# Performance work log

Hardware: AMD Instinct MI355X
Metric: run time of the kernel (lower is better)

The kernel has to match this reference:

```python
import jax, jax.numpy as jnp
import numpy as np

B, H, C, W = 16, 256, 128, 128  # input is (B, H, C_in, W); C_out = C_in = 128


def setup_inputs() -> dict:
    key = jax.random.key(0)
    ks = jax.random.split(key, 7)
    s = 0.02
    return {
        "x": jax.random.normal(ks[0], (B, H, C, W), dtype=jnp.float32),
        "Wq": jax.random.normal(ks[1], (C, C), dtype=jnp.float32) * s,
        "bq": jnp.zeros((C,), dtype=jnp.float32),
        "Wk": jax.random.normal(ks[2], (C, C), dtype=jnp.float32) * s,
        "bk": jnp.zeros((C,), dtype=jnp.float32),
        "Wv": jax.random.normal(ks[3], (C, C), dtype=jnp.float32) * s,
        "bv": jnp.zeros((C,), dtype=jnp.float32),
        "Wn": jax.random.normal(ks[4], (C, C), dtype=jnp.float32) * s,
        "bn": jnp.zeros((C,), dtype=jnp.float32),
        "Wo": jax.random.normal(ks[5], (C, C), dtype=jnp.float32) * s,
        "bo": jnp.zeros((C,), dtype=jnp.float32),
    }


def reference(x, Wq, bq, Wk, bk, Wv, bv, Wn, bn, Wo, bo):
    # x: (B, H, C, W) -> channels_first layout (B, C, H, W)
    xt = jnp.transpose(x, (0, 2, 1, 3))
    # 1x1 channels_first convs == channel-mixing GEMMs
    q = jnp.einsum('bchw,cd->bdhw', xt, Wq) + bq[None, :, None, None]
    k = jnp.einsum('bchw,cd->bdhw', xt, Wk) + bk[None, :, None, None]
    v = jnp.einsum('bchw,cd->bdhw', xt, Wv) + bv[None, :, None, None]
    # QK^T over H, laid out as (B, C, C', W); scale by sqrt(W) (= last dim of k)
    scale = jnp.sqrt(jnp.asarray(k.shape[-1], dtype=x.dtype))
    scores = jnp.einsum('bchw,bdhw->bcdw', q, k) / scale
    attn = jax.nn.softmax(scores, axis=-1)  # softmax over W axis (as in source)
    # DropConnect: identity at inference (training=None)
    # weight_norm: channels_last 1x1 conv mixing the second C axis
    wn = jnp.einsum('bcdw,de->bcew', attn, Wn) + bn[None, None, :, None]
    # attention-value matmul: out[b,c,h,w] = sum_d wn[b,c,d,w] * v[b,d,h,w]
    m = jnp.einsum('bcdw,bdhw->bchw', wn, v)
    # conv1: channels_first 1x1, C_in -> C_out
    out = jnp.einsum('bchw,co->bohw', m, Wo) + bo[None, :, None, None]
    # back to (B, H, C_out, W)
    return jnp.transpose(out, (0, 2, 1, 3))
```

## Files before the change

kernel.cpp:

```cpp
#include <hip/hip_runtime.h>
#include <cstddef>

#define BB 16
#define HH 256
#define CC 128
#define WW 128

typedef _Float16 f16;
typedef _Float16 f16x8 __attribute__((ext_vector_type(8)));
typedef _Float16 f16x4 __attribute__((ext_vector_type(4)));
typedef _Float16 f16x2 __attribute__((ext_vector_type(2)));
typedef float f32x4 __attribute__((ext_vector_type(4)));

#define LD1 136
#define LDX 264
#define REG 17920

__device__ __forceinline__ void zero_acc(f32x4 acc[4][4]) {
#pragma unroll
    for (int i = 0; i < 4; ++i)
#pragma unroll
        for (int j = 0; j < 4; ++j) acc[i][j] = (f32x4){0.f, 0.f, 0.f, 0.f};
}

__device__ __forceinline__ void gemm_ab(const f16* __restrict__ A, int lda,
                                        const f16* __restrict__ B, int ldb,
                                        int K, int m0, int n0, int l15, int quad,
                                        f32x4 acc[4][4]) {
    for (int kc = 0; kc < K; kc += 32) {
        f16x8 af[4], bf[4];
        const f16* ap = A + (size_t)(m0 + l15) * lda + kc + quad * 8;
        const f16* bp = B + (size_t)(n0 + l15) * ldb + kc + quad * 8;
#pragma unroll
        for (int t = 0; t < 4; ++t) {
            af[t] = *(const f16x8*)(ap + t * 16 * lda);
            bf[t] = *(const f16x8*)(bp + t * 16 * ldb);
        }
#pragma unroll
        for (int mt = 0; mt < 4; ++mt)
#pragma unroll
            for (int nt = 0; nt < 4; ++nt)
                acc[mt][nt] = __builtin_amdgcn_mfma_f32_16x16x32_f16(af[mt], bf[nt], acc[mt][nt], 0, 0, 0);
    }
}

__device__ __forceinline__ void gemm_a_btr(const f16* __restrict__ A, int lda,
                                           const f16* __restrict__ XS,
                                           int m0, int n0, int l15, int quad,
                                           f32x4 acc[4][4]) {
    const unsigned xb = (unsigned)(size_t)XS;
    for (int kc = 0; kc < 128; kc += 32) {
        f16x8 af[4];
        const f16* ap = A + (size_t)(m0 + l15) * lda + kc + quad * 8;
#pragma unroll
        for (int t = 0; t < 4; ++t) af[t] = *(const f16x8*)(ap + t * 16 * lda);
        int i0 = (kc >> 2) + 2 * quad;
        f16x4 blo[4], bhi[4];
#pragma unroll
        for (int nt = 0; nt < 4; ++nt) {
            unsigned idx0 = (unsigned)(i0 * 8 + (n0 >> 4) + nt);
            unsigned a0 = xb + (idx0 * 68u + (unsigned)l15 * 4u) * 2u;
            unsigned a1 = a0 + 8u * 68u * 2u;
            asm volatile("ds_read_b64_tr_b16 %0, %1" : "=v"(blo[nt]) : "v"(a0));
            asm volatile("ds_read_b64_tr_b16 %0, %1" : "=v"(bhi[nt]) : "v"(a1));
        }
        asm volatile("s_waitcnt lgkmcnt(0)" ::: "memory");
        __builtin_amdgcn_sched_barrier(0);
#pragma unroll
        for (int nt = 0; nt < 4; ++nt) {
            f16x8 bv = __builtin_shufflevector(blo[nt], bhi[nt], 0, 1, 2, 3, 4, 5, 6, 7);
#pragma unroll
            for (int mt = 0; mt < 4; ++mt)
                acc[mt][nt] = __builtin_amdgcn_mfma_f32_16x16x32_f16(af[mt], bv, acc[mt][nt], 0, 0, 0);
        }
    }
}

__device__ __forceinline__ void stage_ct(const f32x4 acc[4][4], f16* dst, int ld,
                                         int m0, int n0, int l15, int quad) {
#pragma unroll
    for (int mt = 0; mt < 4; ++mt)
#pragma unroll
        for (int nt = 0; nt < 4; ++nt) {
            f16x4 v;
#pragma unroll
            for (int r = 0; r < 4; ++r) v[r] = (f16)acc[mt][nt][r];
            int col = n0 + nt * 16 + l15;
            int row = m0 + mt * 16 + quad * 4;
            *(f16x4*)(dst + (size_t)col * ld + row) = v;
        }
}

__device__ __forceinline__ void stage_ct_r1(const f32x4 acc[4][4], f16* dst, int ld,
                                            int m0, int n0, int l15, int quad,
                                            const float* __restrict__ gv,
                                            const float* __restrict__ wv) {
#pragma unroll
    for (int mt = 0; mt < 4; ++mt)
#pragma unroll
        for (int nt = 0; nt < 4; ++nt) {
            int col = n0 + nt * 16 + l15;
            int row0 = m0 + mt * 16 + quad * 4;
            float ws = wv[col];
            f16x4 v;
#pragma unroll
            for (int r = 0; r < 4; ++r) v[r] = (f16)(acc[mt][nt][r] + ws * gv[row0 + r]);
            *(f16x4*)(dst + (size_t)col * ld + row0) = v;
        }
}

__device__ __forceinline__ void stage_w(const f16* __restrict__ g, f16* dst, int tid) {
#pragma unroll
    for (int i = 0; i < 8; ++i) {
        int idx = tid + i * 256;
        int row = idx >> 4, cc = (idx & 15) * 8;
        *(f16x8*)(dst + row * LD1 + cc) = *(const f16x8*)(g + row * 128 + cc);
    }
}

__global__ __launch_bounds__(256) void prep_w(const float* __restrict__ Wq, const float* __restrict__ Wk,
                                              const float* __restrict__ Wo, f16* __restrict__ out) {
    int id = blockIdx.x * 256 + threadIdx.x;
    int m = id >> 14;
    int r = (id >> 7) & 127, c = id & 127;
    if (m == 0)      out[id] = (f16)Wq[c * 128 + r];
    else if (m == 1) out[id] = (f16)Wk[c * 128 + r];
    else             out[4 * 16384 + (id & 16383)] = (f16)Wo[c * 128 + r];
}

__global__ __launch_bounds__(512) void prep_mv(const float* __restrict__ Wn, const float* __restrict__ Wv,
                                               const float* __restrict__ Wo, const float* __restrict__ bn,
                                               const float* __restrict__ bv,
                                               f16* __restrict__ Wpk, float* __restrict__ Vg) {
    __shared__ f16 As[128 * LD1];
    __shared__ f16 Bs[128 * LD1];
    const int tid = threadIdx.x;
    if (tid < 128) {
        float s = 0.f;
        for (int e = 0; e < 128; ++e) s = fmaf(Wn[tid * 128 + e], bv[e], s);
        Vg[tid] = s;
    } else if (tid < 256) {
        int c = tid - 128;
        float s = 0.f;
        for (int e = 0; e < 128; ++e) s = fmaf(bn[e], Wv[c * 128 + e], s);
        Vg[128 + c] = s;
    } else if (tid < 384) {
        int o = tid - 256;
        float s = 0.f;
        for (int c = 0; c < 128; ++c) s += Wo[c * 128 + o];
        Vg[256 + o] = s;
    } else if (tid == 384) {
        float s = 0.f;
        for (int e = 0; e < 128; ++e) s = fmaf(bn[e], bv[e], s);
        Vg[384] = s;
    }
    if (tid < 256) {
#pragma unroll
        for (int i = 0; i < 8; ++i) {
            int idx = tid + i * 256;
            int r = idx >> 4, c = (idx & 15) * 8;
            f16x8 va, vb;
            const float* pa = Wv + r * 128 + c;
            const float* pb = Wn + r * 128 + c;
#pragma unroll
            for (int j = 0; j < 8; ++j) { va[j] = (f16)pa[j]; vb[j] = (f16)pb[j]; }
            *(f16x8*)(As + r * LD1 + c) = va;
            *(f16x8*)(Bs + r * LD1 + c) = vb;
        }
    }
    __syncthreads();
    if (tid < 256) {
        const int lane = tid & 63, wid = tid >> 6;
        const int l15 = lane & 15, quad = lane >> 4;
        const int m0 = (wid >> 1) * 64, n0 = (wid & 1) * 64;
        f32x4 acc[4][4];
        zero_acc(acc);
        gemm_ab(As, LD1, Bs, LD1, 128, m0, n0, l15, quad, acc);
        f16* Mt = Wpk + 2 * 16384;
#pragma unroll
        for (int mt = 0; mt < 4; ++mt)
#pragma unroll
            for (int r = 0; r < 4; ++r) {
                int cp = m0 + mt * 16 + quad * 4 + r;
#pragma unroll
                for (int nt = 0; nt < 4; ++nt) {
                    int d = n0 + nt * 16 + l15;
                    Mt[cp * 128 + d] = (f16)acc[mt][nt][r];
                }
            }
    }
}

__global__ __launch_bounds__(256) void t1_k(const float* __restrict__ src, f16* __restrict__ dst) {
    __shared__ float tile[32][33];
    int bx = blockIdx.x;
    const int qt = bx & 3;  bx >>= 2;
    const int pt = bx & 7;  bx >>= 3;
    const int c  = bx & 127;
    const int b  = bx >> 7;
    const int tx = threadIdx.x & 31, ty = threadIdx.x >> 5;
    size_t sbase = (((size_t)b * HH + pt * 32) * CC + c) * WW + qt * 32;
#pragma unroll
    for (int k = 0; k < 4; ++k) {
        int i = ty + 8 * k;
        tile[i][tx] = src[sbase + (size_t)i * CC * WW + tx];
    }
    __syncthreads();
    size_t dbase = (((size_t)b * WW + qt * 32) * CC + c) * HH + pt * 32;
#pragma unroll
    for (int k = 0; k < 4; ++k) {
        int i = ty + 8 * k;
        dst[dbase + (size_t)i * CC * HH + tx] = (f16)tile[tx][i];
    }
}

__global__ __launch_bounds__(256) void t2_k(const f16* __restrict__ src, float* __restrict__ dst) {
    __shared__ float tile[32][33];
    int bx = blockIdx.x;
    const int ht = bx & 7;  bx >>= 3;
    const int wt = bx & 3;  bx >>= 2;
    const int c  = bx & 127;
    const int b  = bx >> 7;
    const int tx = threadIdx.x & 31, ty = threadIdx.x >> 5;
    size_t sbase = (((size_t)b * WW + wt * 32) * CC + c) * HH + ht * 32;
#pragma unroll
    for (int k = 0; k < 4; ++k) {
        int i = ty + 8 * k;
        tile[i][tx] = (float)src[sbase + (size_t)i * CC * HH + tx];
    }
    __syncthreads();
    size_t dbase = (((size_t)b * HH + ht * 32) * CC + c) * WW + wt * 32;
#pragma unroll
    for (int k = 0; k < 4; ++k) {
        int i = ty + 8 * k;
        dst[dbase + (size_t)i * CC * WW + tx] = tile[tx][i];
    }
}

__global__ __launch_bounds__(256, 2) void p1_kernel(const f16* __restrict__ Xt,
                                                    const f16* __restrict__ Wpk,
                                                    const float* __restrict__ Wq_g, const float* __restrict__ bq,
                                                    const float* __restrict__ Wk_g, const float* __restrict__ bk,
                                                    f16* __restrict__ Sout) {
    __shared__ f16 sm[2 * REG];
    __shared__ float rbuf[128], rqb[128], rkb[128];
    const int tid = threadIdx.x;
    const int w = blockIdx.x, b = blockIdx.y;
    const f16* Xg = Xt + (size_t)(b * WW + w) * (CC * HH);
    f16* Xs = sm;
    f16* RA = sm;
    f16* RB = sm + REG;

#pragma unroll
    for (int i = 0; i < 16; ++i) {
        int g = tid + i * 256;
        int row = g >> 5, cc = (g & 31) * 8;
        *(f16x8*)(Xs + row * LDX + cc) = *(const f16x8*)(Xg + row * 256 + cc);
    }
    __syncthreads();

    const int lane = tid & 63, wid = tid >> 6;
    const int l15 = lane & 15, quad = lane >> 4;
    const int m0 = (wid >> 1) * 64, n0 = (wid & 1) * 64;

    if (tid < 128) {
        float s = 0.f;
        for (int hc = 0; hc < 32; ++hc) {
            f16x8 v = *(const f16x8*)(Xs + tid * LDX + hc * 8);
#pragma unroll
            for (int j = 0; j < 8; ++j) s += (float)v[j];
        }
        rbuf[tid] = s;
    }

    f32x4 acc[4][4];
    zero_acc(acc);
    gemm_ab(Xs, LDX, Xs, LDX, 256, m0, n0, l15, quad, acc);
    __syncthreads();

    stage_ct(acc, RA, LD1, m0, n0, l15, quad);
    stage_w(Wpk + 0 * 16384, RB, tid);
    if (tid < 128) {
        float s = 0.f;
        for (int c = 0; c < 128; ++c) s = fmaf(Wq_g[c * 128 + tid], rbuf[c], s);
        rqb[tid] = s;
    } else {
        int d = tid - 128;
        float s = 0.f;
        for (int c = 0; c < 128; ++c) s = fmaf(Wk_g[c * 128 + d], rbuf[c], s);
        rkb[d] = s;
    }
    __syncthreads();

    zero_acc(acc);
    gemm_ab(RA, LD1, RB, LD1, 128, m0, n0, l15, quad, acc);
    __syncthreads();
    stage_ct(acc, RA, LD1, m0, n0, l15, quad);
    stage_w(Wpk + 1 * 16384, RB, tid);
    __syncthreads();

    zero_acc(acc);
    gemm_ab(RA, LD1, RB, LD1, 128, m0, n0, l15, quad, acc);

    const float inv_scale = 0.08838834764831845f;
    f16* Sg = Sout + (size_t)(b * WW + w) * (CC * CC);
#pragma unroll
    for (int mt = 0; mt < 4; ++mt)
#pragma unroll
        for (int r = 0; r < 4; ++r) {
            int dq = m0 + mt * 16 + quad * 4 + r;
            float q1 = bq[dq], q2 = rqb[dq];
#pragma unroll
            for (int nt = 0; nt < 4; ++nt) {
                int dk = n0 + nt * 16 + l15;
                float kb = bk[dk], kr = rkb[dk];
                Sg[dq * 128 + dk] = (f16)((acc[mt][nt][r] + q2 * kb + q1 * kr + 256.f * q1 * kb) * inv_scale);
            }
        }
}

__global__ __launch_bounds__(256) void p2_kernel(const f16* __restrict__ S,
                                                 float* __restrict__ z) {
    int i = (blockIdx.x * 256 + threadIdx.x) * 2;
    int b = i >> 14, cd = i & 16383;
    const f16* p = S + (size_t)b * WW * CC * CC + cd;
    float m0v = -1e30f, l0 = 0.f, m1v = -1e30f, l1 = 0.f;
    for (int w = 0; w < WW; ++w) {
        f16x2 sv = *(const f16x2*)(p + (size_t)w * CC * CC);
        float s0 = (float)sv[0], s1 = (float)sv[1];
        if (s0 > m0v) { l0 = fmaf(l0, __expf(m0v - s0), 1.f); m0v = s0; }
        else          { l0 += __expf(s0 - m0v); }
        if (s1 > m1v) { l1 = fmaf(l1, __expf(m1v - s1), 1.f); m1v = s1; }
        else          { l1 += __expf(s1 - m1v); }
    }
    z[i]     = m0v + __logf(l0);
    z[i + 1] = m1v + __logf(l1);
}

__global__ __launch_bounds__(256, 2) void p3_kernel(f16* __restrict__ XtO,
                                                    const f16* __restrict__ Sin, const float* __restrict__ Zin,
                                                    const f16* __restrict__ Wpk,
                                                    const float* __restrict__ Vg,
                                                    const float* __restrict__ bo_g) {
    __shared__ f16 sm[2 * REG];
    __shared__ float t1b[128], ub[128], gb[128], wb[128];
    const int tid = threadIdx.x;
    const int w = blockIdx.x, b = blockIdx.y;
    const f16* Sg = Sin + (size_t)(b * WW + w) * (CC * CC);
    const float* Zb = Zin + (size_t)b * (CC * CC);
    f16* Xg = XtO + (size_t)(b * WW + w) * (CC * HH);
    f16* R0 = sm;
    f16* R1 = sm + REG;

    if (tid < 128) { gb[tid] = Vg[128 + tid]; wb[tid] = Vg[256 + tid]; }

#pragma unroll
    for (int i = 0; i < 16; ++i) {
        int g = tid + i * 256;
        int c = g >> 5, d4 = (g & 31) * 4;
        f16x4 s4 = *(const f16x4*)(Sg + c * 128 + d4);
        float4 z4 = *(const float4*)(Zb + c * 128 + d4);
        f16x4 e;
        e[0] = (f16)__expf((float)s4[0] - z4.x);
        e[1] = (f16)__expf((float)s4[1] - z4.y);
        e[2] = (f16)__expf((float)s4[2] - z4.z);
        e[3] = (f16)__expf((float)s4[3] - z4.w);
        *(f16x4*)(R0 + c * LD1 + d4) = e;
    }
    stage_w(Wpk + 2 * 16384, R1, tid);
    __syncthreads();

    const int lane = tid & 63, wid = tid >> 6;
    const int l15 = lane & 15, quad = lane >> 4;
    const int m0 = (wid >> 1) * 64, n0 = (wid & 1) * 64;

    if (tid < 128) {
        float s = Vg[384];
        for (int d = 0; d < 128; ++d) s = fmaf((float)R0[tid * LD1 + d], Vg[d], s);
        t1b[tid] = s;
    }

    f32x4 acc[4][4];
    zero_acc(acc);
    gemm_ab(R0, LD1, R1, LD1, 128, m0, n0, l15, quad, acc);
    __syncthreads();
    stage_ct(acc, R0, LD1, m0, n0, l15, quad);
    stage_w(Wpk + 4 * 16384, R1, tid);
    __syncthreads();
    if (tid < 128) {
        float s = 0.f;
        for (int c = 0; c < 128; ++c) s = fmaf((float)R1[tid * LD1 + c], t1b[c], s);
        ub[tid] = s + bo_g[tid];
    }
    zero_acc(acc);
    gemm_ab(R0, LD1, R1, LD1, 128, m0, n0, l15, quad, acc);
    __syncthreads();
    stage_ct_r1(acc, R1, LD1, m0, n0, l15, quad, gb, wb);
#pragma unroll
    for (int i = 0; i < 16; ++i) {
        int g = tid + i * 256;
        int c2 = g >> 5, cc = (g & 31) * 4;
        int off = ((c2 >> 2) * 8 + (cc >> 4)) * 68 + (c2 & 3) * 16 + (cc & 12);
        *(f16x4*)(R0 + off) = *(const f16x4*)(Xg + c2 * 256 + cc);
    }
    __syncthreads();
    zero_acc(acc);
    gemm_a_btr(R1, LD1, R0, m0, n0, l15, quad, acc);
#pragma unroll
    for (int mt = 0; mt < 4; ++mt)
#pragma unroll
        for (int r = 0; r < 4; ++r) {
            int o = m0 + mt * 16 + quad * 4 + r;
            float u = ub[o];
#pragma unroll
            for (int nt = 0; nt < 4; ++nt) {
                int h = n0 + nt * 16 + l15;
                Xg[o * 256 + h] = (f16)(acc[mt][nt][r] + u);
            }
        }
    __syncthreads();
#pragma unroll
    for (int i = 0; i < 16; ++i) {
        int g = tid + i * 256;
        int c2 = g >> 5, cc = (g & 31) * 4;
        int off = ((c2 >> 2) * 8 + (cc >> 4)) * 68 + (c2 & 3) * 16 + (cc & 12);
        *(f16x4*)(R0 + off) = *(const f16x4*)(Xg + c2 * 256 + 128 + cc);
    }
    __syncthreads();
    zero_acc(acc);
    gemm_a_btr(R1, LD1, R0, m0, n0, l15, quad, acc);
#pragma unroll
    for (int mt = 0; mt < 4; ++mt)
#pragma unroll
        for (int r = 0; r < 4; ++r) {
            int o = m0 + mt * 16 + quad * 4 + r;
            float u = ub[o];
#pragma unroll
            for (int nt = 0; nt < 4; ++nt) {
                int h = n0 + nt * 16 + l15;
                Xg[o * 256 + 128 + h] = (f16)(acc[mt][nt][r] + u);
            }
        }
}

extern "C" void kernel_launch(void* const* d_in, const int* in_sizes, int n_in,
                              void* d_out, int out_size, void* d_ws, size_t ws_size,
                              hipStream_t stream) {
    const float* x  = (const float*)d_in[0];
    const float* Wq = (const float*)d_in[1];
    const float* bq = (const float*)d_in[2];
    const float* Wk = (const float*)d_in[3];
    const float* bk = (const float*)d_in[4];
    const float* Wv = (const float*)d_in[5];
    const float* bv = (const float*)d_in[6];
    const float* Wn = (const float*)d_in[7];
    const float* bn = (const float*)d_in[8];
    const float* Wo = (const float*)d_in[9];
    const float* bo = (const float*)d_in[10];
    float* out = (float*)d_out;

    f16*   wsX = (f16*)d_ws;
    f16*   wsS = (f16*)((char*)d_ws + 134217728);
    float* wsV = (float*)((char*)d_ws + 134217728 + 67108864);
    float* wsZ = (float*)((char*)d_ws + 268435456);
    f16*   wsW = (f16*)((char*)d_ws + 268435456 + 1048576);

    prep_w<<<192, 256, 0, stream>>>(Wq, Wk, Wo, wsW);
    prep_mv<<<1, 512, 0, stream>>>(Wn, Wv, Wo, bn, bv, wsW, wsV);
    t1_k<<<BB * CC * 8 * 4, 256, 0, stream>>>(x, wsX);
    p1_kernel<<<dim3(WW, BB), 256, 0, stream>>>(wsX, wsW, Wq, bq, Wk, bk, wsS);
    p2_kernel<<<(BB * CC * CC) / 512, 256, 0, stream>>>(wsS, wsZ);
    p3_kernel<<<dim3(WW, BB), 256, 0, stream>>>(wsX, wsS, wsZ, wsW, wsV, bo);
    t2_k<<<BB * CC * 4 * 8, 256, 0, stream>>>(wsX, out);
}
```

Measured before the change: 732.9 us.

## Vectorize transposes, exploit Gram symmetry, prefetch weights into registers, restructure softmax

The transpose kernels now use 64x64 tiles with float4 and f16x8 vector accesses. p3 writes its output in a (w,h,c) layout, and t2 reads that layout so its loads are contiguous. p1 relies on the symmetry of X·X^T: one wave computes the row sums while another mirrors its tile, and both the Wk and Wo weights are prefetched into registers before they are needed. The p2 log-sum-exp loop is unrolled four ways with branchless updates, and p3's exp staging uses 8-wide vectors. In exchange the change adds register pressure and more intricate index math. The mirrored tiles must exactly cover the lower triangle of the Gram matrix.

```diff
diff --git a/kernel.cpp b/kernel.cpp
--- a/kernel.cpp
+++ b/kernel.cpp
@@ -91,6 +91,19 @@
         }
 }
 
+__device__ __forceinline__ void stage_c_mirror(const f32x4 acc[4][4], f16* dst, int ld,
+                                               int m0, int n0, int l15, int quad) {
+#pragma unroll
+    for (int mt = 0; mt < 4; ++mt)
+#pragma unroll
+        for (int r = 0; r < 4; ++r) {
+            int row = m0 + mt * 16 + quad * 4 + r;
+#pragma unroll
+            for (int nt = 0; nt < 4; ++nt)
+                dst[(size_t)row * ld + n0 + nt * 16 + l15] = (f16)acc[mt][nt][r];
+        }
+}
+
 __device__ __forceinline__ void stage_ct_r1(const f32x4 acc[4][4], f16* dst, int ld,
                                             int m0, int n0, int l15, int quad,
                                             const float* __restrict__ gv,
@@ -115,6 +128,41 @@
         int idx = tid + i * 256;
         int row = idx >> 4, cc = (idx & 15) * 8;
         *(f16x8*)(dst + row * LD1 + cc) = *(const f16x8*)(g + row * 128 + cc);
+    }
+}
+
+__device__ __forceinline__ void load_w_reg(const f16* __restrict__ g, f16x8 wr[8], int tid) {
+#pragma unroll
+    for (int i = 0; i < 8; ++i) {
+        int idx = tid + i * 256;
+        wr[i] = *(const f16x8*)(g + (idx >> 4) * 128 + (idx & 15) * 8);
+    }
+}
+__device__ __forceinline__ void stage_w_from_reg(const f16x8 wr[8], f16* dst, int tid) {
+#pragma unroll
+    for (int i = 0; i < 8; ++i) {
+        int idx = tid + i * 256;
+        *(f16x8*)(dst + (idx >> 4) * LD1 + (idx & 15) * 8) = wr[i];
+    }
+}
+__device__ __forceinline__ void load_x_reg(const f16* __restrict__ g, f16x8 wr[8], int tid) {
+#pragma unroll
+    for (int i = 0; i < 8; ++i) {
+        int idx = tid + i * 256;
+        wr[i] = *(const f16x8*)(g + (idx >> 4) * 256 + (idx & 15) * 8);
+    }
+}
+__device__ __forceinline__ void stage_x_from_reg(const f16x8 wr[8], f16* dst, int tid) {
+#pragma unroll
+    for (int i = 0; i < 8; ++i) {
+        int idx = tid + i * 256;
+        int c2 = idx >> 4, cc = (idx & 15) * 8;
+        int off = ((c2 >> 2) * 8 + (cc >> 4)) * 68 + (c2 & 3) * 16 + (cc & 15);
+        f16x4 lo, hi;
+#pragma unroll
+        for (int j = 0; j < 4; ++j) { lo[j] = wr[i][j]; hi[j] = wr[i][4 + j]; }
+        *(f16x4*)(dst + off) = lo;
+        *(f16x4*)(dst + off + 4) = hi;
     }
 }
 
@@ -192,48 +240,67 @@
 }
 
 __global__ __launch_bounds__(256) void t1_k(const float* __restrict__ src, f16* __restrict__ dst) {
-    __shared__ float tile[32][33];
+    __shared__ float tile[64][68];
     int bx = blockIdx.x;
-    const int qt = bx & 3;  bx >>= 2;
-    const int pt = bx & 7;  bx >>= 3;
+    const int pw = bx & 1;  bx >>= 1;
+    const int ph = bx & 3;  bx >>= 2;
     const int c  = bx & 127;
     const int b  = bx >> 7;
-    const int tx = threadIdx.x & 31, ty = threadIdx.x >> 5;
-    size_t sbase = (((size_t)b * HH + pt * 32) * CC + c) * WW + qt * 32;
-#pragma unroll
-    for (int k = 0; k < 4; ++k) {
-        int i = ty + 8 * k;
-        tile[i][tx] = src[sbase + (size_t)i * CC * WW + tx];
-    }
-    __syncthreads();
-    size_t dbase = (((size_t)b * WW + qt * 32) * CC + c) * HH + pt * 32;
-#pragma unroll
-    for (int k = 0; k < 4; ++k) {
-        int i = ty + 8 * k;
-        dst[dbase + (size_t)i * CC * HH + tx] = (f16)tile[tx][i];
+    const int tid = threadIdx.x;
+    const int h0 = ph * 64, w0 = pw * 64;
+    {
+        const int r = tid >> 4, c4 = (tid & 15) * 4;
+        size_t base = (((size_t)b * HH + h0 + r) * CC + c) * WW + w0 + c4;
+#pragma unroll
+        for (int k = 0; k < 4; ++k) {
+            float4 v = *(const float4*)(src + base + (size_t)(16 * k) * CC * WW);
+            *(float4*)&tile[r + 16 * k][c4] = v;
+        }
+    }
+    __syncthreads();
+    {
+        const int rw = tid >> 3, h8 = (tid & 7) * 8;
+        size_t dbase = (((size_t)b * WW + w0 + rw) * CC + c) * HH + h0 + h8;
+#pragma unroll
+        for (int k = 0; k < 2; ++k) {
+            f16x8 v;
+#pragma unroll
+            for (int j = 0; j < 8; ++j) v[j] = (f16)tile[h8 + j][rw + 32 * k];
+            *(f16x8*)(dst + dbase + (size_t)(32 * k) * CC * HH) = v;
+        }
     }
 }
 
 __global__ __launch_bounds__(256) void t2_k(const f16* __restrict__ src, float* __restrict__ dst) {
-    __shared__ float tile[32][33];
+    __shared__ float tile[64][68];
     int bx = blockIdx.x;
-    const int ht = bx & 7;  bx >>= 3;
-    const int wt = bx & 3;  bx >>= 2;
-    const int c  = bx & 127;
-    const int b  = bx >> 7;
-    const int tx = threadIdx.x & 31, ty = threadIdx.x >> 5;
-    size_t sbase = (((size_t)b * WW + wt * 32) * CC + c) * HH + ht * 32;
-#pragma unroll
-    for (int k = 0; k < 4; ++k) {
-        int i = ty + 8 * k;
-        tile[i][tx] = (float)src[sbase + (size_t)i * CC * HH + tx];
-    }
-    __syncthreads();
-    size_t dbase = (((size_t)b * HH + ht * 32) * CC + c) * WW + wt * 32;
-#pragma unroll
-    for (int k = 0; k < 4; ++k) {
-        int i = ty + 8 * k;
-        dst[dbase + (size_t)i * CC * WW + tx] = tile[tx][i];
+    const int ct = bx & 1;  bx >>= 1;
+    const int wt = bx & 1;  bx >>= 1;
+    const int h  = bx & 255;
+    const int b  = bx >> 8;
+    const int tid = threadIdx.x;
+    const int c0 = ct * 64, w0 = wt * 64;
+    {
+        const int r = tid >> 3, c8 = (tid & 7) * 8;
+#pragma unroll
+        for (int k = 0; k < 2; ++k) {
+            int wr = r + 32 * k;
+            f16x8 v = *(const f16x8*)(src + (((size_t)b * WW + w0 + wr) * HH + h) * CC + c0 + c8);
+#pragma unroll
+            for (int j = 0; j < 8; ++j) tile[wr][c8 + j] = (float)v[j];
+        }
+    }
+    __syncthreads();
+    {
+        const int rc = tid >> 4, w4 = (tid & 15) * 4;
+#pragma unroll
+        for (int k = 0; k < 4; ++k) {
+            int cr = rc + 16 * k;
+            float4 o;
+            o.x = tile[w4 + 0][cr]; o.y = tile[w4 + 1][cr];
+            o.z = tile[w4 + 2][cr]; o.w = tile[w4 + 3][cr];
+            *(float4*)(dst + (((size_t)b * HH + h) * CC + c0 + cr) * WW + w0 + w4) = o;
+        }
     }
 }
 
@@ -251,6 +318,9 @@
     f16* RA = sm;
     f16* RB = sm + REG;
 
+    f16x8 wkreg[8];
+    load_w_reg(Wpk + 1 * 16384, wkreg, tid);
+
 #pragma unroll
     for (int i = 0; i < 16; ++i) {
         int g = tid + i * 256;
@@ -263,22 +333,27 @@
     const int l15 = lane & 15, quad = lane >> 4;
     const int m0 = (wid >> 1) * 64, n0 = (wid & 1) * 64;
 
-    if (tid < 128) {
-        float s = 0.f;
-        for (int hc = 0; hc < 32; ++hc) {
-            f16x8 v = *(const f16x8*)(Xs + tid * LDX + hc * 8);
-#pragma unroll
-            for (int j = 0; j < 8; ++j) s += (float)v[j];
-        }
-        rbuf[tid] = s;
-    }
-
     f32x4 acc[4][4];
-    zero_acc(acc);
-    gemm_ab(Xs, LDX, Xs, LDX, 256, m0, n0, l15, quad, acc);
-    __syncthreads();
-
-    stage_ct(acc, RA, LD1, m0, n0, l15, quad);
+    if (wid != 2) {
+        zero_acc(acc);
+        gemm_ab(Xs, LDX, Xs, LDX, 256, m0, n0, l15, quad, acc);
+    } else {
+#pragma unroll
+        for (int hf = 0; hf < 2; ++hf) {
+            int c = lane + 64 * hf;
+            float s = 0.f;
+            for (int hc = 0; hc < 32; ++hc) {
+                f16x8 v = *(const f16x8*)(Xs + (size_t)c * LDX + hc * 8);
+#pragma unroll
+                for (int j = 0; j < 8; ++j) s += (float)v[j];
+            }
+            rbuf[c] = s;
+        }
+    }
+    __syncthreads();
+
+    if (wid != 2) stage_ct(acc, RA, LD1, m0, n0, l15, quad);
+    if (wid == 1) stage_c_mirror(acc, RA, LD1, m0, n0, l15, quad);
     stage_w(Wpk + 0 * 16384, RB, tid);
     if (tid < 128) {
         float s = 0.f;
@@ -296,7 +371,7 @@
     gemm_ab(RA, LD1, RB, LD1, 128, m0, n0, l15, quad, acc);
     __syncthreads();
     stage_ct(acc, RA, LD1, m0, n0, l15, quad);
-    stage_w(Wpk + 1 * 16384, RB, tid);
+    stage_w_from_reg(wkreg, RB, tid);
     __syncthreads();
 
     zero_acc(acc);
@@ -325,13 +400,19 @@
     int b = i >> 14, cd = i & 16383;
     const f16* p = S + (size_t)b * WW * CC * CC + cd;
     float m0v = -1e30f, l0 = 0.f, m1v = -1e30f, l1 = 0.f;
-    for (int w = 0; w < WW; ++w) {
-        f16x2 sv = *(const f16x2*)(p + (size_t)w * CC * CC);
-        float s0 = (float)sv[0], s1 = (float)sv[1];
-        if (s0 > m0v) { l0 = fmaf(l0, __expf(m0v - s0), 1.f); m0v = s0; }
-        else          { l0 += __expf(s0 - m0v); }
-        if (s1 > m1v) { l1 = fmaf(l1, __expf(m1v - s1), 1.f); m1v = s1; }
-        else          { l1 += __expf(s1 - m1v); }
+    for (int w = 0; w < WW; w += 4) {
+        f16x2 v0 = *(const f16x2*)(p + (size_t)(w + 0) * CC * CC);
+        f16x2 v1 = *(const f16x2*)(p + (size_t)(w + 1) * CC * CC);
+        f16x2 v2 = *(const f16x2*)(p + (size_t)(w + 2) * CC * CC);
+        f16x2 v3 = *(const f16x2*)(p + (size_t)(w + 3) * CC * CC);
+#pragma unroll
+        for (int j = 0; j < 4; ++j) {
+            f16x2 v = (j == 0) ? v0 : (j == 1) ? v1 : (j == 2) ? v2 : v3;
+            float s0 = (float)v[0], s1 = (float)v[1];
+            float n0 = fmaxf(m0v, s0), n1 = fmaxf(m1v, s1);
+            l0 = fmaf(l0, __expf(m0v - n0), __expf(s0 - n0)); m0v = n0;
+            l1 = fmaf(l1, __expf(m1v - n1), __expf(s1 - n1)); m1v = n1;
+        }
     }
     z[i]     = m0v + __logf(l0);
     z[i + 1] = m1v + __logf(l1);
@@ -352,20 +433,28 @@
     f16* R0 = sm;
     f16* R1 = sm + REG;
 
+    f16x8 wreg[8];
+    load_w_reg(Wpk + 4 * 16384, wreg, tid);
+
     if (tid < 128) { gb[tid] = Vg[128 + tid]; wb[tid] = Vg[256 + tid]; }
 
 #pragma unroll
-    for (int i = 0; i < 16; ++i) {
+    for (int i = 0; i < 8; ++i) {
         int g = tid + i * 256;
-        int c = g >> 5, d4 = (g & 31) * 4;
-        f16x4 s4 = *(const f16x4*)(Sg + c * 128 + d4);
-        float4 z4 = *(const float4*)(Zb + c * 128 + d4);
-        f16x4 e;
-        e[0] = (f16)__expf((float)s4[0] - z4.x);
-        e[1] = (f16)__expf((float)s4[1] - z4.y);
-        e[2] = (f16)__expf((float)s4[2] - z4.z);
-        e[3] = (f16)__expf((float)s4[3] - z4.w);
-        *(f16x4*)(R0 + c * LD1 + d4) = e;
+        int c = g >> 4, d8 = (g & 15) * 8;
+        f16x8 s8 = *(const f16x8*)(Sg + c * 128 + d8);
+        float4 za = *(const float4*)(Zb + c * 128 + d8);
+        float4 zc = *(const float4*)(Zb + c * 128 + d8 + 4);
+        f16x8 e;
+        e[0] = (f16)__expf((float)s8[0] - za.x);
+        e[1] = (f16)__expf((float)s8[1] - za.y);
+        e[2] = (f16)__expf((float)s8[2] - za.z);
+        e[3] = (f16)__expf((float)s8[3] - za.w);
+        e[4] = (f16)__expf((float)s8[4] - zc.x);
+        e[5] = (f16)__expf((float)s8[5] - zc.y);
+        e[6] = (f16)__expf((float)s8[6] - zc.z);
+        e[7] = (f16)__expf((float)s8[7] - zc.w);
+        *(f16x8*)(R0 + c * LD1 + d8) = e;
     }
     stage_w(Wpk + 2 * 16384, R1, tid);
     __syncthreads();
@@ -385,7 +474,8 @@
     gemm_ab(R0, LD1, R1, LD1, 128, m0, n0, l15, quad, acc);
     __syncthreads();
     stage_ct(acc, R0, LD1, m0, n0, l15, quad);
-    stage_w(Wpk + 4 * 16384, R1, tid);
+    stage_w_from_reg(wreg, R1, tid);
+    load_x_reg(Xg, wreg, tid);
     __syncthreads();
     if (tid < 128) {
         float s = 0.f;
@@ -396,50 +486,37 @@
     gemm_ab(R0, LD1, R1, LD1, 128, m0, n0, l15, quad, acc);
     __syncthreads();
     stage_ct_r1(acc, R1, LD1, m0, n0, l15, quad, gb, wb);
-#pragma unroll
-    for (int i = 0; i < 16; ++i) {
-        int g = tid + i * 256;
-        int c2 = g >> 5, cc = (g & 31) * 4;
-        int off = ((c2 >> 2) * 8 + (cc >> 4)) * 68 + (c2 & 3) * 16 + (cc & 12);
-        *(f16x4*)(R0 + off) = *(const f16x4*)(Xg + c2 * 256 + cc);
-    }
+    stage_x_from_reg(wreg, R0, tid);
+    load_x_reg(Xg + 128, wreg, tid);
     __syncthreads();
     zero_acc(acc);
     gemm_a_btr(R1, LD1, R0, m0, n0, l15, quad, acc);
 #pragma unroll
     for (int mt = 0; mt < 4; ++mt)
 #pragma unroll
-        for (int r = 0; r < 4; ++r) {
-            int o = m0 + mt * 16 + quad * 4 + r;
-            float u = ub[o];
-#pragma unroll
-            for (int nt = 0; nt < 4; ++nt) {
-                int h = n0 + nt * 16 + l15;
-                Xg[o * 256 + h] = (f16)(acc[mt][nt][r] + u);
-            }
-        }
-    __syncthreads();
-#pragma unroll
-    for (int i = 0; i < 16; ++i) {
-        int g = tid + i * 256;
-        int c2 = g >> 5, cc = (g & 31) * 4;
-        int off = ((c2 >> 2) * 8 + (cc >> 4)) * 68 + (c2 & 3) * 16 + (cc & 12);
-        *(f16x4*)(R0 + off) = *(const f16x4*)(Xg + c2 * 256 + 128 + cc);
-    }
+        for (int nt = 0; nt < 4; ++nt) {
+            int h = n0 + nt * 16 + l15;
+            int o = m0 + mt * 16 + quad * 4;
+            f16x4 v;
+#pragma unroll
+            for (int r = 0; r < 4; ++r) v[r] = (f16)(acc[mt][nt][r] + ub[o + r]);
+            *(f16x4*)(Xg + h * 128 + o) = v;
+        }
+    __syncthreads();
+    stage_x_from_reg(wreg, R0, tid);
     __syncthreads();
     zero_acc(acc);
     gemm_a_btr(R1, LD1, R0, m0, n0, l15, quad, acc);
 #pragma unroll
     for (int mt = 0; mt < 4; ++mt)
 #pragma unroll
-        for (int r = 0; r < 4; ++r) {
-            int o = m0 + mt * 16 + quad * 4 + r;
-            float u = ub[o];
-#pragma unroll
-            for (int nt = 0; nt < 4; ++nt) {
-                int h = n0 + nt * 16 + l15;
-                Xg[o * 256 + 128 + h] = (f16)(acc[mt][nt][r] + u);
-            }
+        for (int nt = 0; nt < 4; ++nt) {
+            int h = 128 + n0 + nt * 16 + l15;
+            int o = m0 + mt * 16 + quad * 4;
+            f16x4 v;
+#pragma unroll
+            for (int r = 0; r < 4; ++r) v[r] = (f16)(acc[mt][nt][r] + ub[o + r]);
+            *(f16x4*)(Xg + h * 128 + o) = v;
         }
 }
 
@@ -467,9 +544,9 @@
 
     prep_w<<<192, 256, 0, stream>>>(Wq, Wk, Wo, wsW);
     prep_mv<<<1, 512, 0, stream>>>(Wn, Wv, Wo, bn, bv, wsW, wsV);
-    t1_k<<<BB * CC * 8 * 4, 256, 0, stream>>>(x, wsX);
+    t1_k<<<BB * CC * 4 * 2, 256, 0, stream>>>(x, wsX);
     p1_kernel<<<dim3(WW, BB), 256, 0, stream>>>(wsX, wsW, Wq, bq, Wk, bk, wsS);
     p2_kernel<<<(BB * CC * CC) / 512, 256, 0, stream>>>(wsS, wsZ);
     p3_kernel<<<dim3(WW, BB), 256, 0, stream>>>(wsX, wsS, wsZ, wsW, wsV, bo);
-    t2_k<<<BB * CC * 4 * 8, 256, 0, stream>>>(wsX, out);
-}
+    t2_k<<<BB * 256 * 2 * 2, 256, 0, stream>>>(wsX, out);
+}
```

Measured after the change: 691.2 us. 1.06x faster.
